# Performance work log

Hardware: AMD Instinct MI355X
Metric: run time of the kernel (lower is better)

The kernel has to match this reference:

```python
import jax, jax.numpy as jnp
import numpy as np

EPS_OT = 0.05   # sinkhorn epsilon
ITERS = 3       # sinkhorn iterations
NH = 8          # attention heads


def _l2norm(x, axis):
    return x / jnp.maximum(jnp.linalg.norm(x, axis=axis, keepdims=True), 1e-12)


def _conv(x, w, pad):
    return jax.lax.conv_general_dilated(
        x, w, (1, 1), ((pad, pad), (pad, pad)),
        dimension_numbers=("NCHW", "OIHW", "NCHW"))


def _head(x, w1, b1, g, beta, w2, b2):
    # Conv3x3 -> BatchNorm (train-mode batch stats) -> ReLU -> Conv1x1
    h = _conv(x, w1, 1) + b1[None, :, None, None]
    mu = jnp.mean(h, (0, 2, 3), keepdims=True)
    var = jnp.var(h, (0, 2, 3), keepdims=True)
    h = jax.nn.relu((h - mu) / jnp.sqrt(var + 1e-5) * g[None, :, None, None]
                    + beta[None, :, None, None])
    return jnp.einsum("oc,bchw->bohw", w2, h) + b2[None, :, None, None]


def setup_inputs() -> dict:
    key = jax.random.key(0)
    ks = jax.random.split(key, 20)
    B, C, H, W, TD = 8, 256, 48, 48, 512
    s = 0.02
    f32 = jnp.float32
    d = {
        "img_feat": jax.random.normal(ks[0], (B, C, H, W), f32),
        "txt_feat": jax.random.normal(ks[1], (B, TD), f32),
        "density_map": jax.random.uniform(ks[2], (B, 1, H, W), f32),
        "tp_w": s * jax.random.normal(ks[3], (C, TD), f32), "tp_b": jnp.zeros((C,), f32),
        "wq": s * jax.random.normal(ks[4], (C, C), f32), "bq": jnp.zeros((C,), f32),
        "wk": s * jax.random.normal(ks[5], (C, C), f32), "bk": jnp.zeros((C,), f32),
        "wv": s * jax.random.normal(ks[6], (C, C), f32), "bv": jnp.zeros((C,), f32),
        "wo": s * jax.random.normal(ks[7], (C, C), f32), "bo": jnp.zeros((C,), f32),
        "ln_g": jnp.ones((C,), f32), "ln_b": jnp.zeros((C,), f32),
        "op_w": s * jax.random.normal(ks[8], (C, C), f32), "op_b": jnp.zeros((C,), f32),
        "h1_w": s * jax.random.normal(ks[9], (C // 2, C, 3, 3), f32), "h1_b": jnp.zeros((C // 2,), f32),
        "h_bn_g": jnp.ones((C // 2,), f32), "h_bn_b": jnp.zeros((C // 2,), f32),
        "h2_w": s * jax.random.normal(ks[10], (2, C // 2), f32), "h2_b": jnp.zeros((2,), f32),
        "v1_w": s * jax.random.normal(ks[11], (C // 2, C, 3, 3), f32), "v1_b": jnp.zeros((C // 2,), f32),
        "v_bn_g": jnp.ones((C // 2,), f32), "v_bn_b": jnp.zeros((C // 2,), f32),
        "v2_w": s * jax.random.normal(ks[12], (2, C // 2), f32), "v2_b": jnp.zeros((2,), f32),
        "temperature": 0.07 * jnp.ones((1,), f32),
        "spatial_weight": 0.1 * jnp.ones((1,), f32),
    }
    return d


def reference(img_feat, txt_feat, density_map, tp_w, tp_b, wq, bq, wk, bk,
              wv, bv, wo, bo, ln_g, ln_b, op_w, op_b, h1_w, h1_b, h_bn_g,
              h_bn_b, h2_w, h2_b, v1_w, v1_b, v_bn_g, v_bn_b, v2_w, v2_b,
              temperature, spatial_weight):
    B, C, H, W = img_feat.shape
    N = H * W
    hd = C // NH

    # ---- text projection (single text token) ----
    txt_emb = txt_feat @ tp_w.T + tp_b                      # [B,C]

    # ---- cross attention: query = pixels, key/value = 1 text token ----
    img_flat = img_feat.reshape(B, C, N).transpose(0, 2, 1)  # [B,N,C]
    q = (img_flat @ wq.T + bq).reshape(B, N, NH, hd)
    k = (txt_emb @ wk.T + bk).reshape(B, 1, NH, hd)
    v = (txt_emb @ wv.T + bv).reshape(B, 1, NH, hd)
    scores = jnp.einsum("bnhd,bkhd->bhnk", q, k) / jnp.sqrt(jnp.float32(hd))
    attn = jax.nn.softmax(scores, axis=-1)                  # ones (k len = 1)
    ctx = jnp.einsum("bhnk,bkhd->bnhd", attn, v).reshape(B, N, C)
    attn_out = ctx @ wo.T + bo

    # ---- residual + layernorm ----
    x = img_flat + attn_out
    mu = jnp.mean(x, -1, keepdims=True)
    var = jnp.var(x, -1, keepdims=True)
    source_feat = (x - mu) / jnp.sqrt(var + 1e-5) * ln_g + ln_b   # [B,N,C]
    mod_img_feat = source_feat.transpose(0, 2, 1).reshape(B, C, H, W)

    # ---- target distribution q from density map ----
    target = jax.nn.relu(density_map.reshape(B, N)) + 1e-6
    q_dist = target / jnp.sum(target, axis=1, keepdims=True)

    # ---- source distribution p from cosine similarity ----
    img_n = _l2norm(mod_img_feat, 1)                        # [B,C,H,W]
    txt_n = _l2norm(txt_emb, 1)                             # [B,C]
    cos = jnp.sum(img_n * txt_n[:, :, None, None], axis=1).reshape(B, N)
    temp = jnp.clip(temperature, 0.01, None)                # [1]
    logits = cos / temp
    mask = (cos > 0.0).astype(jnp.float32)
    shifted = logits - jnp.max(logits, axis=1, keepdims=True)
    p_un = jnp.exp(shifted) * mask + 1e-8
    p = p_un / jnp.sum(p_un, axis=1, keepdims=True)

    # ---- cost matrix: feature + spatial ----
    src_n = _l2norm(source_feat, 2)                         # [B,N,C]
    feature_cost = 1.0 - jnp.einsum("bnc,bmc->bnm", src_n, src_n)
    gy, gx = jnp.meshgrid(jnp.linspace(0.0, 1.0, H), jnp.linspace(0.0, 1.0, W),
                          indexing="ij")
    coords = jnp.stack([gy, gx], -1).reshape(N, 2)
    d2 = jnp.sum((coords[:, None, :] - coords[None, :, :]) ** 2, -1)
    spatial_cost = jnp.sqrt(jnp.maximum(d2, 0.0)) / 1.41421356  # [N,N]
    cost = feature_cost + spatial_weight * spatial_cost[None]   # [B,N,N]

    # ---- log-domain Sinkhorn ----
    log_p = jnp.log(p + 1e-12)
    log_q = jnp.log(q_dist + 1e-12)
    f = jnp.zeros_like(p)
    g = jnp.zeros_like(q_dist)
    for _ in range(ITERS):
        f = EPS_OT * (log_p - jax.scipy.special.logsumexp(
            (g[:, None, :] - cost) / EPS_OT, axis=2))
        g = EPS_OT * (log_q - jax.scipy.special.logsumexp(
            (f[:, :, None] - cost) / EPS_OT, axis=1))
    T = jnp.exp((f[:, :, None] + g[:, None, :] - cost) / EPS_OT)

    # ---- transport features: T^T @ source ----
    fused = jnp.einsum("bnm,bnc->bmc", T, source_feat)      # [B,N,C]
    fused_feat = fused.transpose(0, 2, 1).reshape(B, C, H, W)

    out_feat = img_feat + (jnp.einsum("oc,bchw->bohw", op_w, fused_feat)
                           + op_b[None, :, None, None])
    heatmap_logits = _head(out_feat, h1_w, h1_b, h_bn_g, h_bn_b, h2_w, h2_b)
    hv_logits = _head(out_feat, v1_w, v1_b, v_bn_g, v_bn_b, v2_w, v2_b)
    return out_feat, heatmap_logits, hv_logits
```

## Files before the change

kernel.cpp:

```cpp
#include <hip/hip_runtime.h>
#include <hip/hip_bf16.h>

#define NTOK 2304
#define CCH  256
#define BB   8
#define NSPL 2

typedef __attribute__((ext_vector_type(4))) float f32x4;
typedef __attribute__((ext_vector_type(8))) short s16x8;
typedef __attribute__((ext_vector_type(8))) _Float16 h16x8;
typedef unsigned short u16;
typedef unsigned char u8;

__device__ __forceinline__ u16 f2bf(float x){
  union{float f; unsigned u;} v; v.f = x;
  unsigned r = v.u + 0x7fffu + ((v.u>>16)&1u);
  return (u16)(r>>16);
}
__device__ __forceinline__ float bf2f(u16 h){
  union{float f; unsigned u;} v; v.u = ((unsigned)h)<<16; return v.f;
}

#if __has_builtin(__builtin_amdgcn_cvt_f32_fp8) && __has_builtin(__builtin_amdgcn_cvt_pk_fp8_f32)
#define HWFP8 1
#else
#define HWFP8 0
#endif

__device__ __forceinline__ u8 enc8(float z){
  union{float f; unsigned u;} a; a.f = fabsf(z) * 0x1p-120f;
  unsigned u = a.u + 0x7FFFFu + ((a.u>>20)&1u);
  unsigned b = (u>>20)&0x7Fu;
  if (b > 0x7Eu) b = 0x7Eu;
  return (u8)(b | (z<0.f ? 0x80u : 0u));
}
__device__ __forceinline__ float dec8(unsigned b){
  union{unsigned u; float f;} w;
  w.u = ((b&0x80u)<<24) | ((b&0x7Fu)<<20);
  return w.f * 0x1p120f;
}

#if HWFP8
__device__ __forceinline__ float DEC8(unsigned w, int e){
  switch(e & 3){
    case 0:  return __builtin_amdgcn_cvt_f32_fp8((int)w, 0);
    case 1:  return __builtin_amdgcn_cvt_f32_fp8((int)w, 1);
    case 2:  return __builtin_amdgcn_cvt_f32_fp8((int)w, 2);
    default: return __builtin_amdgcn_cvt_f32_fp8((int)w, 3);
  }
}
__device__ __forceinline__ unsigned pack4(float z0,float z1,float z2,float z3){
  int v = __builtin_amdgcn_cvt_pk_fp8_f32(z0, z1, 0, false);
  v = __builtin_amdgcn_cvt_pk_fp8_f32(z2, z3, v, true);
  return (unsigned)v;
}
#else
__device__ __forceinline__ float DEC8(unsigned w, int e){
  return dec8((w>>(8*(e&3)))&0xFFu);
}
__device__ __forceinline__ unsigned pack4(float z0,float z1,float z2,float z3){
  return (unsigned)enc8(z0) | ((unsigned)enc8(z1)<<8) |
         ((unsigned)enc8(z2)<<16) | ((unsigned)enc8(z3)<<24);
}
#endif

__device__ __forceinline__ int swz512(int row, int b){ return row*512 + (b ^ ((row&7)<<4)); }
__device__ __forceinline__ int swz128(int row, int b){ return row*128 + (b ^ ((row&7)<<4)); }
__device__ __forceinline__ int swz64 (int row, int b){ return row*64  + (b ^ ((row&3)<<4)); }

__device__ __forceinline__ void gl_lds16(const void* g, void* l){
  __builtin_amdgcn_global_load_lds(
      (const __attribute__((address_space(1))) unsigned int*)g,
      (__attribute__((address_space(3))) unsigned int*)l, 16, 0, 0);
}

struct CanonArgs {
  const void* src[31];
  int n[31];
  int off[31];
};

__global__ void k_detect(const u16* probe, int* flag){
  if (threadIdx.x==0){
    int cnt=0;
    for (int i=0;i<16;++i){
      unsigned e = (probe[2*i]>>7)&0xFFu;
      if (e>=100u && e<=140u) ++cnt;
    }
    *flag = (cnt>=14)?1:0;
  }
}

__global__ __launch_bounds__(256) void k_canon(CanonArgs a, float* dst, const int* flag, int nt){
  int t = blockIdx.y;
  if (t>=nt) return;
  int n = a.n[t];
  const void* s = a.src[t];
  float* d = dst + a.off[t];
  bool isbf = (*flag)!=0;
  int n4 = n >> 2;
  for (int i = blockIdx.x*256+threadIdx.x; i < n4; i += gridDim.x*256){
    if (isbf){
      ushort4 v = ((const ushort4*)s)[i];
      float4 o; o.x=bf2f(v.x); o.y=bf2f(v.y); o.z=bf2f(v.z); o.w=bf2f(v.w);
      ((float4*)d)[i] = o;
    } else {
      ((float4*)d)[i] = ((const float4*)s)[i];
    }
  }
  int base = n4<<2;
  int rem = n - base;
  int i = blockIdx.x*256+threadIdx.x;
  if (i < rem)
    d[base+i] = isbf ? bf2f(((const u16*)s)[base+i]) : ((const float*)s)[base+i];
}

__global__ __launch_bounds__(256) void k_zero(float* p, int n4){
  int i = blockIdx.x*256+threadIdx.x;
  if (i < n4) ((float4*)p)[i] = (float4){0.f,0.f,0.f,0.f};
}

__global__ __launch_bounds__(256) void k_txt(const float* txt, const float* tpw, const float* tpb,
    const float* wv, const float* bv, const float* wo, const float* bo, float* TXTN, float* AVEC){
  int b=blockIdx.x, t=threadIdx.x;
  __shared__ float sT[512];
  __shared__ float sE[256];
  __shared__ float sV[256];
  __shared__ float red[4];
  sT[t]      = txt[b*512+t];
  sT[t+256]  = txt[b*512+256+t];
  __syncthreads();
  float acc = tpb[t];
  const float* wr = tpw + (size_t)t*512;
  for (int k=0;k<512;++k) acc = fmaf(sT[k], wr[k], acc);
  sE[t] = acc;
  float ss = acc*acc;
  for (int d=1; d<64; d<<=1) ss += __shfl_xor(ss, d);
  if ((t&63)==0) red[t>>6] = ss;
  __syncthreads();
  float nrm = sqrtf(red[0]+red[1]+red[2]+red[3]);
  TXTN[b*256+t] = acc / fmaxf(nrm, 1e-12f);
  float av = bv[t];
  const float* wvr = wv + (size_t)t*256;
  for (int k=0;k<256;++k) av = fmaf(sE[k], wvr[k], av);
  sV[t] = av;
  __syncthreads();
  float ao = bo[t];
  const float* wor = wo + (size_t)t*256;
  for (int k=0;k<256;++k) ao = fmaf(sV[k], wor[k], ao);
  AVEC[b*256+t] = ao;
}

__global__ __launch_bounds__(256) void k_lnfuse(const float* img, const float* AVEC, const float* lng,
    const float* lnb, const float* TXTN, u16* SF, u16* SN, float* COS){
  int b=blockIdx.y, n0=blockIdx.x*32, t=threadIdx.x;
  __shared__ float xt[32][256];
  float av = AVEC[b*256+t];
  const float* ip = img + ((size_t)b*256 + t)*NTOK + n0;
  #pragma unroll
  for (int j4=0;j4<8;++j4){
    float4 v = *(const float4*)(ip + j4*4);
    xt[j4*4+0][t]=v.x+av; xt[j4*4+1][t]=v.y+av; xt[j4*4+2][t]=v.z+av; xt[j4*4+3][t]=v.w+av;
  }
  int wv_=t>>6, l=t&63;
  float lg[4], lb[4], tn[4];
  #pragma unroll
  for (int k=0;k<4;++k){ lg[k]=lng[l+64*k]; lb[k]=lnb[l+64*k]; tn[k]=TXTN[b*256+l+64*k]; }
  __syncthreads();
  for (int rr=0; rr<8; ++rr){
    int j = wv_*8+rr; int n = n0+j;
    float x[4]; float s=0.f, ss=0.f;
    #pragma unroll
    for (int k=0;k<4;++k){ float v=xt[j][l+64*k]; x[k]=v; s+=v; ss=fmaf(v,v,ss); }
    for (int d=1; d<64; d<<=1){ s += __shfl_xor(s,d); ss += __shfl_xor(ss,d); }
    float mu = s*(1.f/256.f);
    float var = ss*(1.f/256.f) - mu*mu;
    float rstd = rsqrtf(fmaxf(var,0.f)+1e-5f);
    float y[4]; float sy=0.f;
    #pragma unroll
    for (int k=0;k<4;++k){ y[k] = fmaf((x[k]-mu)*rstd, lg[k], lb[k]); sy = fmaf(y[k],y[k],sy); }
    for (int d=1; d<64; d<<=1) sy += __shfl_xor(sy,d);
    float rn = 1.f/fmaxf(sqrtf(sy),1e-12f);
    float cp = 0.f;
    size_t base = ((size_t)b*NTOK + n)*CCH;
    #pragma unroll
    for (int k=0;k<4;++k){
      float sv = y[k]*rn;
      SF[base + l+64*k] = f2bf(y[k]);
      SN[base + l+64*k] = f2bf(sv);
      cp = fmaf(sv, tn[k], cp);
    }
    for (int d=1; d<64; d<<=1) cp += __shfl_xor(cp,d);
    if (l==0) COS[b*NTOK+n] = cp;
  }
}

__global__ __launch_bounds__(256) void k_pqred(const float* COS, const float* den, const float* tmpp, float* PQS){
  int b=blockIdx.x, t=threadIdx.x;
  __shared__ float red[256];
  float temp = fmaxf(tmpp[0], 0.01f);
  float mx = -1e30f;
  for (int n=t; n<NTOK; n+=256) mx = fmaxf(mx, COS[b*NTOK+n]);
  red[t]=mx; __syncthreads();
  for (int o=128;o>0;o>>=1){ if (t<o) red[t]=fmaxf(red[t],red[t+o]); __syncthreads(); }
  float maxc = red[0]; __syncthreads();
  float sp=0.f, st=0.f;
  for (int n=t; n<NTOK; n+=256){
    float cv = COS[b*NTOK+n];
    sp += __expf((cv-maxc)/temp)*((cv>0.f)?1.f:0.f)+1e-8f;
    float dv = den[b*NTOK+n];
    st += fmaxf(dv,0.f)+1e-6f;
  }
  red[t]=sp; __syncthreads();
  for (int o=128;o>0;o>>=1){ if (t<o) red[t]+=red[t+o]; __syncthreads(); }
  sp = red[0]; __syncthreads();
  red[t]=st; __syncthreads();
  for (int o=128;o>0;o>>=1){ if (t<o) red[t]+=red[t+o]; __syncthreads(); }
  if (t==0){ PQS[b*4]=maxc; PQS[b*4+1]=sp; PQS[b*4+2]=red[0]; }
}

__global__ __launch_bounds__(256) void k_pqelem(const float* COS, const float* den, const float* tmpp,
    const float* swp, const float* PQS, float* LOGP, float* LOGQ, float* GV, u16* PJ, float* SPT){
  int idx = blockIdx.x*256+threadIdx.x;
  float temp = fmaxf(tmpp[0], 0.01f);
  if (idx < BB*NTOK){
    int b = idx / NTOK;
    float maxc = PQS[b*4], sp = PQS[b*4+1], st = PQS[b*4+2];
    float cv = COS[idx];
    float pu = __expf((cv-maxc)/temp)*((cv>0.f)?1.f:0.f)+1e-8f;
    LOGP[idx] = logf(pu/sp + 1e-12f);
    float dv = den[idx];
    LOGQ[idx] = logf((fmaxf(dv,0.f)+1e-6f)/st + 1e-12f);
    GV[idx] = 0.f;
  }
  if (idx < NTOK){
    int h = idx/48, w = idx - h*48;
    PJ[idx] = (u16)(h*95 + w);
  }
  if (idx < 9025){
    int dh = idx/95 - 47, dw = idx - (idx/95)*95 - 47;
    float spw = swp[0]*(20.0f/1.41421356f);
    float dy = (float)dh*(1.f/47.f), dx = (float)dw*(1.f/47.f);
    SPT[idx] = spw*sqrtf(fmaf(dy,dy,dx*dx));
  }
}

__global__ __launch_bounds__(256) void k_packw(const float* h1w, const float* v1w, u16* W2P){
  int idx = blockIdx.x*256+threadIdx.x;
  int kc = idx >> 14;
  int rem = idx & 16383;
  int o = rem >> 6;
  int cl = rem & 63;
  int tap = kc >> 2;
  int c = ((kc&3)<<6) + cl;
  int head = o >> 7, oc = o & 127;
  const float* src = head ? v1w : h1w;
  W2P[idx] = f2bf(src[(oc*256 + c)*9 + tap]);
}

__global__ __launch_bounds__(256) void k_trans(const u16* SF, u16* SFT){
  int n0 = blockIdx.x*64, c0 = blockIdx.y*64, b = blockIdx.z;
  __shared__ u16 tl[64][68];
  int t = threadIdx.x;
  int nl = t>>3, c8 = (t&7)*8;
  #pragma unroll
  for (int p=0;p<2;++p){
    int n = nl + p*32;
    s16x8 v = *(const s16x8*)(SF + ((size_t)(b*NTOK + n0+n)*CCH + c0 + c8));
    #pragma unroll
    for (int e=0;e<8;++e) tl[c8+e][n] = (u16)v[e];
  }
  __syncthreads();
  int cl = t>>3, n8 = (t&7)*8;
  #pragma unroll
  for (int p=0;p<2;++p){
    int c = cl + p*32;
    union{ s16x8 v; u16 us[8]; } pk;
    #pragma unroll
    for (int e=0;e<8;++e){ int s = n8+e; pk.us[e] = tl[c][((s&3)<<4) | (s>>2)]; }
    *(s16x8*)(SFT + ((size_t)(b*CCH + c0+c)*NTOK + n0 + n8)) = pk.v;
  }
}

__global__ __launch_bounds__(256, 5) void k_cost(const u16* SN, const u16* PJ, const float* SPT,
    u8* Z, float* PZ, int b_base){
  int zb = blockIdx.z, b = b_base + zb;
  int i0 = blockIdx.x*64, by = blockIdx.y, j0b = by*256;
  const u16* SNb = SN + (size_t)b*NTOK*CCH;
  u8* Zb = Z + (size_t)zb*NTOK*NTOK;
  __shared__ __align__(16) char Bs[64*512];
  int tid=threadIdx.x, w=tid>>6, l=tid&63, g4=l>>4, lc=l&15;
  const u16* Arow = SNb + (size_t)(i0 + w*16 + lc)*CCH + g4*8;
  s16x8 af[8];
  #pragma unroll
  for (int ks=0; ks<8; ++ks) af[ks] = *(const s16x8*)(Arow + ks*32);
  int mrow = w*16 + g4*4;
  int ipi[4];
  #pragma unroll
  for (int r=0;r<4;++r) ipi[r] = (int)PJ[i0+mrow+r] + 4512;
  float Srow[4] = {0.f,0.f,0.f,0.f};
  auto STAGE = [&](int js){
    int j0 = j0b + js*64;
    #pragma unroll
    for (int u=0; u<8; ++u){
      int row = u*8 + w*2 + (l>>5);
      int src = ((l&31)*16) ^ ((row&7)<<4);
      gl_lds16((const char*)(SNb + (size_t)(j0+row)*CCH) + src, Bs + u*4096 + w*1024);
    }
  };
  STAGE(0);
  __syncthreads();
  for (int js=0; js<4; ++js){
    int j0 = j0b + js*64;
    f32x4 acc[4];
    #pragma unroll
    for (int cf=0;cf<4;++cf) acc[cf] = (f32x4){0.f,0.f,0.f,0.f};
    #pragma unroll
    for (int ks=0; ks<8; ++ks){
      int kb = ks*64 + g4*16;
      #pragma unroll
      for (int cf=0; cf<4; ++cf){
        s16x8 bb = *(const s16x8*)(Bs + swz512(cf*16+lc, kb));
        acc[cf] = __builtin_amdgcn_mfma_f32_16x16x32_bf16(af[ks], bb, acc[cf], 0,0,0);
      }
    }
    __builtin_amdgcn_sched_barrier(0);
    __builtin_amdgcn_s_barrier();
    __builtin_amdgcn_sched_barrier(0);
    if (js < 3) STAGE(js+1);
    __builtin_amdgcn_sched_barrier(0);
    float zf[4][4];
    #pragma unroll
    for (int cf=0; cf<4; ++cf){
      int j = j0 + cf*16 + lc;
      int pjj = (int)PJ[j];
      #pragma unroll
      for (int r=0;r<4;++r){
        float sp = SPT[ipi[r] - pjj];
        zf[cf][r] = (acc[cf][r]-1.0f)*20.0f - sp;
      }
    }
    size_t zrow = (size_t)(i0+mrow)*NTOK + j0 + lc*4;
    #pragma unroll
    for (int r=0;r<4;++r){
      unsigned pw = pack4(zf[0][r], zf[1][r], zf[2][r], zf[3][r]);
      Srow[r] += __expf(DEC8(pw,0)) + __expf(DEC8(pw,1))
               + __expf(DEC8(pw,2)) + __expf(DEC8(pw,3));
      *(unsigned*)(Zb + zrow + (size_t)r*NTOK) = pw;
    }
    __builtin_amdgcn_sched_barrier(0);
    __builtin_amdgcn_s_barrier();
    __builtin_amdgcn_sched_barrier(0);
  }
  #pragma unroll
  for (int r=0;r<4;++r){
    float s = Srow[r];
    s += __shfl_xor(s,1); s += __shfl_xor(s,2); s += __shfl_xor(s,4); s += __shfl_xor(s,8);
    if (lc==0) PZ[(size_t)(zb*NTOK + i0 + mrow + r)*9 + by] = s;
  }
}

__global__ __launch_bounds__(256) void k_sinkred(const float* PZ, const float* LOGP, float* FV,
    int b_base, int zcnt){
  int idx = blockIdx.x*256 + threadIdx.x;
  if (idx >= zcnt*NTOK) return;
  int zb = idx / NTOK, row = idx - zb*NTOK, b = b_base + zb;
  const float* p = PZ + (size_t)idx*9;
  float s = 0.f;
  #pragma unroll
  for (int k=0;k<9;++k) s += p[k];
  FV[b*NTOK+row] = 0.05f*(LOGP[b*NTOK+row] - logf(s));
}

__global__ __launch_bounds__(256) void k_sinkZ(const u8* Z, const float* addv,
    const float* basev, float* outv, int b_base){
  int zb = blockIdx.y, b = b_base + zb, i0 = blockIdx.x*32;
  __shared__ float fs[NTOK];
  __shared__ float wm[4];
  int t = threadIdx.x;
  for (int j=t; j<NTOK; j+=256){
    int p = j & 63, tt = ((p&3)<<4) | (p>>2);
    fs[j] = addv[b*NTOK + (j & ~63) + tt]*20.f;
  }
  __syncthreads();
  float m = -1e30f;
  for (int j=t; j<NTOK; j+=256) m = fmaxf(m, fs[j]);
  #pragma unroll
  for (int d=1; d<64; d<<=1) m = fmaxf(m, __shfl_xor(m, d));
  if ((t&63)==0) wm[t>>6] = m;
  __syncthreads();
  float C = fmaxf(fmaxf(wm[0],wm[1]), fmaxf(wm[2],wm[3]));
  __syncthreads();
  for (int j=t; j<NTOK; j+=256) fs[j] -= C;
  __syncthreads();
  int rl = t>>3, q = t&7;
  int row = i0 + rl;
  const u8* zr = Z + ((size_t)zb*NTOK + row)*NTOK;
  float S = 0.f;
  for (int c0 = q*32; c0 < NTOK; c0 += 256){
    uint4 zA = *(const uint4*)(zr + c0);
    uint4 zB = *(const uint4*)(zr + c0 + 16);
    unsigned wd[8] = {zA.x,zA.y,zA.z,zA.w, zB.x,zB.y,zB.z,zB.w};
    float s32 = 0.f;
    #pragma unroll
    for (int k=0;k<8;++k)
      #pragma unroll
      for (int e=0;e<4;++e)
        s32 += __expf(fs[c0 + k*4 + e] + DEC8(wd[k], e));
    S += s32;
  }
  #pragma unroll
  for (int d=1; d<8; d<<=1) S += __shfl_xor(S, d);
  if (q==0)
    outv[b*NTOK+row] = 0.05f*(basev[b*NTOK+row] - (C + logf(S)));
}

__global__ __launch_bounds__(256, 3) void k_applyT(const u8* Z, const u16* SFT, const float* FVv,
    const float* GVv, float* FUF, int b_base){
  int zb = blockIdx.z, b = b_base + zb, m0 = blockIdx.x*64;
  int sp = blockIdx.y;
  int nbeg = sp*(NTOK/NSPL), nend = nbeg + (NTOK/NSPL);
  __shared__ __align__(16) char WtL[64*128];
  __shared__ __align__(16) char BL[256*128];
  __shared__ float gs[64];
  __shared__ float sfv[NTOK/NSPL];
  int tid=threadIdx.x, w=tid>>6, l=tid&63, g4=l>>4, lc=l&15;
  if (tid<64) gs[tid] = GVv[b*NTOK+m0+tid]*20.f;
  const float* Fv = FVv + b*NTOK;
  for (int j=tid; j<NTOK/NSPL; j+=256){
    int jj = nbeg + j;
    int p = jj & 63, tt = ((p&3)<<4) | (p>>2);
    sfv[j] = Fv[(jj & ~63) + tt]*20.f;
  }
  const u8* Zb = Z + ((size_t)zb*NTOK + m0)*NTOK;
  const u16* SFTb = SFT + (size_t)b*CCH*NTOK;
  f32x4 acc[4][4];
  #pragma unroll
  for (int mf=0;mf<4;++mf)
    #pragma unroll
    for (int cf=0;cf<4;++cf) acc[mf][cf] = (f32x4){0.f,0.f,0.f,0.f};
  int zm = tid>>2, zq = (tid&3)*16;
  int lrow = l>>3;
  int lsrc = ((l&7)*16) ^ (lrow<<4);
  uint4 zwc = *(const uint4*)(Zb + (size_t)zm*NTOK + nbeg + zq);
  for (int n0=nbeg; n0<nend; n0+=64){
    __syncthreads();
    int nn = (n0+64 < nend) ? n0+64 : nbeg;
    uint4 zwn = *(const uint4*)(Zb + (size_t)zm*NTOK + nn + zq);
    #pragma unroll
    for (int u=0; u<8; ++u){
      int row = w*64 + u*8 + lrow;
      gl_lds16((const char*)(SFTb + (size_t)row*NTOK) + n0*2 + lsrc,
               BL + (w*64 + u*8)*128);
    }
    {
      float g20 = gs[zm];
      unsigned wd[4] = {zwc.x, zwc.y, zwc.z, zwc.w};
      union{ s16x8 v; u16 us[8]; } w0, w1;
      int sbase = n0 - nbeg + zq;
      #pragma unroll
      for (int col=0; col<16; ++col){
        float val = __expf(sfv[sbase+col] + g20 + DEC8(wd[col>>2], col&3));
        if (col < 8) w0.us[col] = f2bf(val); else w1.us[col-8] = f2bf(val);
      }
      *(s16x8*)(WtL + swz128(zm, zq*2)) = w0.v;
      *(s16x8*)(WtL + swz128(zm, zq*2+16)) = w1.v;
    }
    __syncthreads();
    #pragma unroll
    for (int kk=0; kk<2; ++kk){
      s16x8 a[4];
      #pragma unroll
      for (int mf=0;mf<4;++mf) a[mf] = *(const s16x8*)(WtL + swz128(mf*16+lc, kk*64 + g4*16));
      #pragma unroll
      for (int cf=0; cf<4; ++cf){
        s16x8 bb = *(const s16x8*)(BL + swz128(w*64+cf*16+lc, kk*64 + g4*16));
        #pragma unroll
        for (int mf=0; mf<4; ++mf)
          acc[mf][cf] = __builtin_amdgcn_mfma_f32_16x16x32_bf16(a[mf], bb, acc[mf][cf], 0,0,0);
      }
    }
    zwc = zwn;
  }
  float* FUb = FUF + (size_t)b*NTOK*CCH;
  #pragma unroll
  for (int mf=0; mf<4; ++mf)
    #pragma unroll
    for (int cf=0; cf<4; ++cf)
      #pragma unroll
      for (int r=0;r<4;++r){
        int m = m0 + mf*16 + g4*4 + r;
        int c = w*64 + cf*16 + lc;
        atomicAdd(&FUb[(size_t)m*CCH + c], acc[mf][cf][r]);
      }
}

__global__ __launch_bounds__(256) void k_opgemm(const float* FUF, const float* opw, const float* opb,
    const float* img, float* dout, u16* OFN){
  int b=blockIdx.y, n0=blockIdx.x*64;
  __shared__ __align__(16) char Am[64*512];
  __shared__ __align__(16) char Bw[256*64];
  int tid=threadIdx.x, w=tid>>6, l=tid&63, g4=l>>4, lc=l&15;
  const float* FUb = FUF + (size_t)b*NTOK*CCH;
  for (int ch=tid; ch<64*32; ch+=256){
    int r=ch>>5, c8=(ch&31)*8;
    const float* fp = FUb + (size_t)(n0+r)*CCH + c8;
    float4 v0 = *(const float4*)fp;
    float4 v1 = *(const float4*)(fp+4);
    union { s16x8 v; u16 us[8]; } pk;
    pk.us[0]=f2bf(v0.x); pk.us[1]=f2bf(v0.y); pk.us[2]=f2bf(v0.z); pk.us[3]=f2bf(v0.w);
    pk.us[4]=f2bf(v1.x); pk.us[5]=f2bf(v1.y); pk.us[6]=f2bf(v1.z); pk.us[7]=f2bf(v1.w);
    *(s16x8*)(Am + swz512(r, c8*2)) = pk.v;
  }
  f32x4 acc[4][4];
  #pragma unroll
  for (int mf=0;mf<4;++mf)
    #pragma unroll
    for (int cf=0;cf<4;++cf) acc[mf][cf] = (f32x4){0.f,0.f,0.f,0.f};
  for (int ks=0; ks<8; ++ks){
    __syncthreads();
    {
      int o = tid;
      const float* wr = opw + (size_t)o*CCH + ks*32;
      #pragma unroll
      for (int u=0; u<4; ++u){
        float4 v0 = *(const float4*)(wr + u*8);
        float4 v1 = *(const float4*)(wr + u*8 + 4);
        union { s16x8 v; u16 us[8]; } pk;
        pk.us[0]=f2bf(v0.x); pk.us[1]=f2bf(v0.y); pk.us[2]=f2bf(v0.z); pk.us[3]=f2bf(v0.w);
        pk.us[4]=f2bf(v1.x); pk.us[5]=f2bf(v1.y); pk.us[6]=f2bf(v1.z); pk.us[7]=f2bf(v1.w);
        *(s16x8*)(Bw + swz64(o, u*16)) = pk.v;
      }
    }
    __syncthreads();
    #pragma unroll
    for (int mf=0; mf<4; ++mf){
      s16x8 a = *(const s16x8*)(Am + swz512(mf*16+lc, (ks*32+g4*8)*2));
      #pragma unroll
      for (int cf=0; cf<4; ++cf){
        int o = w*64+cf*16+lc;
        s16x8 bb = *(const s16x8*)(Bw + swz64(o, g4*16));
        acc[mf][cf] = __builtin_amdgcn_mfma_f32_16x16x32_bf16(a, bb, acc[mf][cf], 0,0,0);
      }
    }
  }
  #pragma unroll
  for (int mf=0; mf<4; ++mf){
    int nl = mf*16 + g4*4; int n = n0+nl;
    #pragma unroll
    for (int cf=0; cf<4; ++cf){
      int o = w*64+cf*16+lc;
      float ob = opb[o];
      const float* ip = img + ((size_t)b*CCH + o)*NTOK + n;
      float4 im = *(const float4*)ip;
      float o0 = acc[mf][cf][0]+ob+im.x;
      float o1 = acc[mf][cf][1]+ob+im.y;
      float o2 = acc[mf][cf][2]+ob+im.z;
      float o3 = acc[mf][cf][3]+ob+im.w;
      float4 st; st.x=o0; st.y=o1; st.z=o2; st.w=o3;
      *(float4*)(dout + ((size_t)b*CCH+o)*NTOK + n) = st;
      u16* ofp = OFN + ((size_t)b*NTOK + n)*CCH + o;
      ofp[0]=f2bf(o0); ofp[CCH]=f2bf(o1); ofp[2*CCH]=f2bf(o2); ofp[3*CCH]=f2bf(o3);
    }
  }
}

__global__ __launch_bounds__(256, 2) void k_conv2(const u16* OFN, const u16* W2P,
    const float* h1b, const float* v1b, u16* H1, u16* H2){
  int b = blockIdx.y, n0 = blockIdx.x*64;
  __shared__ __align__(16) char As[64*128];
  __shared__ __align__(16) char Ws[2][256*128];
  int tid=threadIdx.x, w=tid>>6, l=tid&63, g4=l>>4, lc=l&15;
  int ar = tid>>2, aseg = (tid&3)*16;
  int arow = n0 + ar;
  int hr = arow/48, wc = arow - hr*48;
  const u16* Ob = OFN + (size_t)b*NTOK*CCH;
  int wrow = tid>>3;
  int wsrc = ((tid&7)*16) ^ ((wrow&7)<<4);
  const char* Wbase = (const char*)W2P;
  f32x4 acc[4][4];
  #pragma unroll
  for (int mf=0;mf<4;++mf)
    #pragma unroll
    for (int of=0;of<4;++of) acc[mf][of] = (f32x4){0.f,0.f,0.f,0.f};
  auto STAGEW = [&](int kc, int buf){
    const char* src = Wbase + (size_t)kc*32768;
    #pragma unroll
    for (int u=0; u<8; ++u)
      gl_lds16(src + (size_t)(u*32 + wrow)*128 + wsrc, Ws[buf] + u*4096 + w*1024);
  };
  auto LOADA = [&](int kc, s16x8& ra0, s16x8& ra1){
    int tap = kc>>2, cq = (kc&3)*64;
    int kh = tap/3;
    int dh = kh-1, dw = (tap-kh*3)-1;
    bool val = ((unsigned)(hr+dh) < 48u) && ((unsigned)(wc+dw) < 48u);
    ra0 = (s16x8){0,0,0,0,0,0,0,0}; ra1 = ra0;
    if (val){
      const u16* ap = Ob + (size_t)(arow + dh*48 + dw)*CCH + cq + aseg;
      ra0 = *(const s16x8*)ap;
      ra1 = *(const s16x8*)(ap+8);
    }
  };
  s16x8 a0, a1, na0, na1;
  STAGEW(0, 0);
  LOADA(0, a0, a1);
  for (int kc=0; kc<36; ++kc){
    int cur = kc & 1;
    __builtin_amdgcn_s_barrier();
    __builtin_amdgcn_sched_barrier(0);
    if (kc+1 < 36){
      STAGEW(kc+1, cur^1);
      LOADA(kc+1, na0, na1);
    }
    *(s16x8*)(As + swz128(ar, aseg*2))    = a0;
    *(s16x8*)(As + swz128(ar, aseg*2+16)) = a1;
    asm volatile("s_waitcnt lgkmcnt(0)" ::: "memory");
    __builtin_amdgcn_s_barrier();
    __builtin_amdgcn_sched_barrier(0);
    #pragma unroll
    for (int ks=0; ks<2; ++ks){
      s16x8 af[4];
      #pragma unroll
      for (int mf=0;mf<4;++mf) af[mf] = *(const s16x8*)(As + swz128(mf*16+lc, ks*64 + g4*16));
      #pragma unroll
      for (int of=0; of<4; ++of){
        s16x8 bf = *(const s16x8*)(Ws[cur] + swz128(w*64+of*16+lc, ks*64 + g4*16));
        #pragma unroll
        for (int mf=0; mf<4; ++mf)
          acc[mf][of] = __builtin_amdgcn_mfma_f32_16x16x32_bf16(af[mf], bf, acc[mf][of], 0,0,0);
      }
    }
    a0 = na0; a1 = na1;
  }
  #pragma unroll
  for (int of=0; of<4; ++of){
    int o = w*64 + of*16 + lc;
    int head = o>>7, oc = o&127;
    float bias = (head? v1b : h1b)[oc];
    u16* Hh = head? H2 : H1;
    #pragma unroll
    for (int mf=0; mf<4; ++mf){
      #pragma unroll
      for (int r=0;r<4;++r){
        int n = n0 + mf*16 + g4*4 + r;
        Hh[((size_t)b*NTOK+n)*128 + oc] = f2bf(acc[mf][of][r] + bias);
      }
    }
  }
}

__global__ __launch_bounds__(128) void k_stats(const u16* H1, const u16* H2, float* PART){
  int head=blockIdx.y, blk=blockIdx.x, t=threadIdx.x;
  const u16* Hh = head? H2:H1;
  float s=0.f, ss=0.f;
  size_t r0 = (size_t)blk*288;
  for (int r=0;r<288;++r){
    float v = bf2f(Hh[(r0+r)*128 + t]);
    s += v; ss = fmaf(v,v,ss);
  }
  PART[((head*64+blk)*128+t)*2]   = s;
  PART[((head*64+blk)*128+t)*2+1] = ss;
}

__global__ __launch_bounds__(128) void k_statr(const float* PART, const float* hbg, const float* hbb,
    const float* vbg, const float* vbb, float* BNS){
  int head=blockIdx.x, t=threadIdx.x;
  float s=0.f, ss=0.f;
  for (int blk=0;blk<64;++blk){
    s  += PART[((head*64+blk)*128+t)*2];
    ss += PART[((head*64+blk)*128+t)*2+1];
  }
  float mean = s*(1.f/18432.f);
  float var = ss*(1.f/18432.f) - mean*mean;
  var = fmaxf(var, 0.f);
  const float* g  = head? vbg:hbg;
  const float* be = head? vbb:hbb;
  float sc = g[t]/sqrtf(var+1e-5f);
  BNS[(head*128+t)*2]   = sc;
  BNS[(head*128+t)*2+1] = be[t] - mean*sc;
}

__global__ __launch_bounds__(128) void k_fin(const u16* H1, const u16* H2, const float* BNS,
    const float* h2w, const float* h2b, const float* v2w, const float* v2b, float* dout){
  int head = blockIdx.z, b = blockIdx.y, n0 = blockIdx.x*128, t=threadIdx.x;
  const u16* Hh = head? H2:H1;
  const float* w2 = head? v2w:h2w;
  const float* b2 = head? v2b:h2b;
  __shared__ u16 tile[128][130];
  __shared__ float sc[128], bi[128], wa[128], wb[128];
  sc[t]=BNS[(head*128+t)*2]; bi[t]=BNS[(head*128+t)*2+1];
  wa[t]=w2[t]; wb[t]=w2[128+t];
  for (int r=0;r<128;++r) tile[r][t] = Hh[((size_t)b*NTOK+n0+r)*128 + t];
  __syncthreads();
  float a0=b2[0], a1=b2[1];
  for (int ch=0; ch<128; ++ch){
    float v = fmaf(bf2f(tile[t][ch]), sc[ch], bi[ch]);
    v = fmaxf(v, 0.f);
    a0 = fmaf(wa[ch], v, a0);
    a1 = fmaf(wb[ch], v, a1);
  }
  size_t base = (size_t)8*256*2304 + (size_t)head*36864 + (size_t)b*2*2304 + n0 + t;
  dout[base]        = a0;
  dout[base+2304]   = a1;
}

extern "C" void kernel_launch(void* const* d_in, const int* in_sizes, int n_in,
                              void* d_out, int out_size, void* d_ws, size_t ws_size,
                              hipStream_t stream){
  (void)out_size;
  long off[31]; long tot=0;
  int ni = n_in < 31 ? n_in : 31;
  for (int i=0;i<ni;++i){ off[i]=tot; tot += ((long)in_sizes[i]+63)&~63L; }
  char* ws = (char*)d_ws;
  size_t pos = 0;
  auto alloc = [&](size_t bytes)->char*{
    char* p = ws+pos; pos = (pos + bytes + 255) & ~(size_t)255; return p; };
  int*   FLAG = (int*)alloc(256);
  float* TXTN = (float*)alloc(8*256*4);
  float* AVEC = (float*)alloc(8*256*4);
  float* COS  = (float*)alloc(8*2304*4);
  float* LOGP = (float*)alloc(8*2304*4);
  float* LOGQ = (float*)alloc(8*2304*4);
  float* FV   = (float*)alloc(8*2304*4);
  float* GV   = (float*)alloc(8*2304*4);
  u16*   PJ   = (u16*)alloc(2304*2);
  float* SPT  = (float*)alloc(9025*4);
  float* PQS  = (float*)alloc(8*4*4);
  float* PART = (float*)alloc(2*64*128*2*4);
  float* BNS  = (float*)alloc(2*128*2*4);
  float* PZ   = (float*)alloc((size_t)8*2304*9*4);
  u16* W2P = (u16*)alloc((size_t)36*256*64*2);
  u16* SF  = (u16*)alloc((size_t)8*2304*256*2);
  u16* SN  = (u16*)alloc((size_t)8*2304*256*2);
  u16* SFT = (u16*)alloc((size_t)8*2304*256*2);
  float* FUF = (float*)alloc((size_t)8*2304*256*4);
  u16* OFN = (u16*)alloc((size_t)8*2304*256*2);
  u16* H1  = (u16*)alloc((size_t)8*2304*128*2);
  u16* H2  = (u16*)alloc((size_t)8*2304*128*2);
  float* canon = (float*)alloc((size_t)tot*4);
  size_t zslice = (size_t)NTOK*NTOK;
  int zsl = (pos + 8*zslice + 256 <= ws_size) ? 8 : 1;
  u8* Z = (u8*)alloc((size_t)zsl*zslice);

  k_detect<<<1,64,0,stream>>>((const u16*)d_in[1], FLAG);
  CanonArgs ca;
  for (int i=0;i<ni;++i){ ca.src[i]=d_in[i]; ca.n[i]=in_sizes[i]; ca.off[i]=(int)off[i]; }
  k_canon<<<dim3(512,(unsigned)ni),256,0,stream>>>(ca, canon, FLAG, ni);
  k_zero<<<4608,256,0,stream>>>(FUF, 8*2304*256/4);

  const float* c_img = canon+off[0];
  const float* c_txt = canon+off[1];
  const float* c_den = canon+off[2];
  const float* c_tpw = canon+off[3];
  const float* c_tpb = canon+off[4];
  const float* c_wv  = canon+off[9];
  const float* c_bv  = canon+off[10];
  const float* c_wo  = canon+off[11];
  const float* c_bo  = canon+off[12];
  const float* c_lng = canon+off[13];
  const float* c_lnb = canon+off[14];
  const float* c_opw = canon+off[15];
  const float* c_opb = canon+off[16];
  const float* c_h1w = canon+off[17];
  const float* c_h1b = canon+off[18];
  const float* c_hbg = canon+off[19];
  const float* c_hbb = canon+off[20];
  const float* c_h2w = canon+off[21];
  const float* c_h2b = canon+off[22];
  const float* c_v1w = canon+off[23];
  const float* c_v1b = canon+off[24];
  const float* c_vbg = canon+off[25];
  const float* c_vbb = canon+off[26];
  const float* c_v2w = canon+off[27];
  const float* c_v2b = canon+off[28];
  const float* c_tmp = canon+off[29];
  const float* c_sw  = canon+off[30];

  k_txt<<<8,256,0,stream>>>(c_txt, c_tpw, c_tpb, c_wv, c_bv, c_wo, c_bo, TXTN, AVEC);
  k_lnfuse<<<dim3(72,8),256,0,stream>>>(c_img, AVEC, c_lng, c_lnb, TXTN, SF, SN, COS);
  k_pqred<<<8,256,0,stream>>>(COS, c_den, c_tmp, PQS);
  k_pqelem<<<80,256,0,stream>>>(COS, c_den, c_tmp, c_sw, PQS, LOGP, LOGQ, GV, PJ, SPT);
  k_packw<<<2304,256,0,stream>>>(c_h1w, c_v1w, W2P);
  k_trans<<<dim3(36,4,8),256,0,stream>>>(SF, SFT);

  if (zsl == 8){
    k_cost<<<dim3(36,9,8),256,0,stream>>>(SN, PJ, SPT, Z, PZ, 0);
    k_sinkred<<<72,256,0,stream>>>(PZ, LOGP, FV, 0, 8);
    for (int it=0; it<3; ++it){
      if (it>0) k_sinkZ<<<dim3(72,8),256,0,stream>>>(Z, GV, LOGP, FV, 0);
      k_sinkZ<<<dim3(72,8),256,0,stream>>>(Z, FV, LOGQ, GV, 0);
    }
    k_applyT<<<dim3(36,NSPL,8),256,0,stream>>>(Z, SFT, FV, GV, FUF, 0);
  } else {
    for (int bi=0; bi<8; ++bi){
      k_cost<<<dim3(36,9,1),256,0,stream>>>(SN, PJ, SPT, Z, PZ, bi);
      k_sinkred<<<9,256,0,stream>>>(PZ, LOGP, FV, bi, 1);
      for (int it=0; it<3; ++it){
        if (it>0) k_sinkZ<<<dim3(72,1),256,0,stream>>>(Z, GV, LOGP, FV, bi);
        k_sinkZ<<<dim3(72,1),256,0,stream>>>(Z, FV, LOGQ, GV, bi);
      }
      k_applyT<<<dim3(36,NSPL,1),256,0,stream>>>(Z, SFT, FV, GV, FUF, bi);
    }
  }

  k_opgemm<<<dim3(36,8),256,0,stream>>>(FUF, c_opw, c_opb, c_img, (float*)d_out, OFN);
  k_conv2<<<dim3(36,8),256,0,stream>>>(OFN, W2P, c_h1b, c_v1b, H1, H2);
  k_stats<<<dim3(64,2),128,0,stream>>>(H1, H2, PART);
  k_statr<<<2,128,0,stream>>>(PART, c_hbg, c_hbb, c_vbg, c_vbb, BNS);
  k_fin<<<dim3(18,8,2),128,0,stream>>>(H1, H2, BNS, c_h2w, c_h2b, c_v2w, c_v2b, (float*)d_out);
}
```

Measured before the change: 407.8 us.

## Store cost Z tiles as 16-byte rows with 256-wide column permutation

```diff
diff --git a/kernel.cpp b/kernel.cpp
--- a/kernel.cpp
+++ b/kernel.cpp
@@ -63,6 +63,10 @@
          ((unsigned)enc8(z2)<<16) | ((unsigned)enc8(z3)<<24);
 }
 #endif
+
+__device__ __forceinline__ int unperm256(int s){
+  return (((s>>2)&3)<<6) + ((s&3)<<4) + (s>>4);
+}
 
 __device__ __forceinline__ int swz512(int row, int b){ return row*512 + (b ^ ((row&7)<<4)); }
 __device__ __forceinline__ int swz128(int row, int b){ return row*128 + (b ^ ((row&7)<<4)); }
@@ -259,12 +263,12 @@
 }
 
 __global__ __launch_bounds__(256) void k_trans(const u16* SF, u16* SFT){
-  int n0 = blockIdx.x*64, c0 = blockIdx.y*64, b = blockIdx.z;
-  __shared__ u16 tl[64][68];
+  int n0 = blockIdx.x*256, c0 = blockIdx.y*64, b = blockIdx.z;
+  __shared__ u16 tl[64][260];
   int t = threadIdx.x;
   int nl = t>>3, c8 = (t&7)*8;
   #pragma unroll
-  for (int p=0;p<2;++p){
+  for (int p=0;p<8;++p){
     int n = nl + p*32;
     s16x8 v = *(const s16x8*)(SF + ((size_t)(b*NTOK + n0+n)*CCH + c0 + c8));
     #pragma unroll
@@ -275,10 +279,14 @@
   #pragma unroll
   for (int p=0;p<2;++p){
     int c = cl + p*32;
-    union{ s16x8 v; u16 us[8]; } pk;
-    #pragma unroll
-    for (int e=0;e<8;++e){ int s = n8+e; pk.us[e] = tl[c][((s&3)<<4) | (s>>2)]; }
-    *(s16x8*)(SFT + ((size_t)(b*CCH + c0+c)*NTOK + n0 + n8)) = pk.v;
+    #pragma unroll
+    for (int q=0;q<4;++q){
+      int s0 = q*64 + n8;
+      union{ s16x8 v; u16 us[8]; } pk;
+      #pragma unroll
+      for (int e=0;e<8;++e){ int s = s0+e; pk.us[e] = tl[c][unperm256(s)]; }
+      *(s16x8*)(SFT + ((size_t)(b*CCH + c0+c)*NTOK + n0 + s0)) = pk.v;
+    }
   }
 }
 
@@ -299,6 +307,7 @@
   #pragma unroll
   for (int r=0;r<4;++r) ipi[r] = (int)PJ[i0+mrow+r] + 4512;
   float Srow[4] = {0.f,0.f,0.f,0.f};
+  unsigned pws[4][4];
   auto STAGE = [&](int js){
     int j0 = j0b + js*64;
     #pragma unroll
@@ -310,6 +319,7 @@
   };
   STAGE(0);
   __syncthreads();
+  #pragma unroll
   for (int js=0; js<4; ++js){
     int j0 = j0b + js*64;
     f32x4 acc[4];
@@ -340,17 +350,22 @@
         zf[cf][r] = (acc[cf][r]-1.0f)*20.0f - sp;
       }
     }
-    size_t zrow = (size_t)(i0+mrow)*NTOK + j0 + lc*4;
     #pragma unroll
     for (int r=0;r<4;++r){
       unsigned pw = pack4(zf[0][r], zf[1][r], zf[2][r], zf[3][r]);
       Srow[r] += __expf(DEC8(pw,0)) + __expf(DEC8(pw,1))
                + __expf(DEC8(pw,2)) + __expf(DEC8(pw,3));
-      *(unsigned*)(Zb + zrow + (size_t)r*NTOK) = pw;
+      pws[r][js] = pw;
     }
     __builtin_amdgcn_sched_barrier(0);
     __builtin_amdgcn_s_barrier();
     __builtin_amdgcn_sched_barrier(0);
+  }
+  size_t zbase = (size_t)(i0+mrow)*NTOK + j0b + lc*16;
+  #pragma unroll
+  for (int r=0;r<4;++r){
+    uint4 st; st.x=pws[r][0]; st.y=pws[r][1]; st.z=pws[r][2]; st.w=pws[r][3];
+    *(uint4*)(Zb + zbase + (size_t)r*NTOK) = st;
   }
   #pragma unroll
   for (int r=0;r<4;++r){
@@ -379,8 +394,8 @@
   __shared__ float wm[4];
   int t = threadIdx.x;
   for (int j=t; j<NTOK; j+=256){
-    int p = j & 63, tt = ((p&3)<<4) | (p>>2);
-    fs[j] = addv[b*NTOK + (j & ~63) + tt]*20.f;
+    int s = j & 255;
+    fs[j] = addv[b*NTOK + (j & ~255) + unperm256(s)]*20.f;
   }
   __syncthreads();
   float m = -1e30f;
@@ -429,8 +444,8 @@
   const float* Fv = FVv + b*NTOK;
   for (int j=tid; j<NTOK/NSPL; j+=256){
     int jj = nbeg + j;
-    int p = jj & 63, tt = ((p&3)<<4) | (p>>2);
-    sfv[j] = Fv[(jj & ~63) + tt]*20.f;
+    int s = jj & 255;
+    sfv[j] = Fv[(jj & ~255) + unperm256(s)]*20.f;
   }
   const u8* Zb = Z + ((size_t)zb*NTOK + m0)*NTOK;
   const u16* SFTb = SFT + (size_t)b*CCH*NTOK;
@@ -781,7 +796,7 @@
   k_pqred<<<8,256,0,stream>>>(COS, c_den, c_tmp, PQS);
   k_pqelem<<<80,256,0,stream>>>(COS, c_den, c_tmp, c_sw, PQS, LOGP, LOGQ, GV, PJ, SPT);
   k_packw<<<2304,256,0,stream>>>(c_h1w, c_v1w, W2P);
-  k_trans<<<dim3(36,4,8),256,0,stream>>>(SF, SFT);
+  k_trans<<<dim3(9,4,8),256,0,stream>>>(SF, SFT);
 
   if (zsl == 8){
     k_cost<<<dim3(36,9,8),256,0,stream>>>(SN, PJ, SPT, Z, PZ, 0);
```

New measurement: 395.8 us. 1.03x faster.
